# Kernel optimization log

Measured on AMD Instinct MI355X. Metric: run time of the kernel, lower is better.

## Reference

```python
import jax, jax.numpy as jnp
import numpy as np

D_MODEL = 1024
NUM_ATOMS = 16384
TEMPERATURE = 1.0
NEG_INF = -1e9


def setup_inputs() -> dict:
    key = jax.random.key(0)
    kx, kd, km = jax.random.split(key, 3)
    x = jax.random.normal(kx, (4, 2048, D_MODEL), dtype=jnp.float32)
    # xavier_uniform for [num_atoms, d_model]
    limit = float(np.sqrt(6.0 / (NUM_ATOMS + D_MODEL)))
    dictionary = jax.random.uniform(
        kd, (NUM_ATOMS, D_MODEL), dtype=jnp.float32, minval=-limit, maxval=limit
    )
    mask = jax.random.randint(km, (4, 2048, NUM_ATOMS), 0, 2, dtype=jnp.int32)
    return {"x": x, "dictionary": dictionary, "mask": mask}


def reference(x, dictionary, mask):
    # scores: [b, s, num_atoms]
    scores = jnp.einsum("bsd,ad->bsa", x, dictionary)
    m = mask.astype(scores.dtype)
    scores = scores * m + (1.0 - m) * NEG_INF
    weights = jax.nn.softmax(scores / TEMPERATURE, axis=-1)
    reconstruction = jnp.einsum("bsa,ad->bsd", weights, dictionary)
    argmax_indices = jnp.argmax(scores, axis=-1)
    return reconstruction, argmax_indices
```

## Files before the change

### kernel.cpp

```cpp
#include <hip/hip_runtime.h>

#define NTOK   8192
#define DMODEL 1024
#define NATOM  16384

typedef _Float16 half8  __attribute__((ext_vector_type(8)));
typedef _Float16 half4_t __attribute__((ext_vector_type(4)));
typedef float    f32x4  __attribute__((ext_vector_type(4)));

#define GLOAD_LDS16(gsrc, ldst) \
  __builtin_amdgcn_global_load_lds((const __attribute__((address_space(1))) unsigned int*)(gsrc), \
                                   (__attribute__((address_space(3))) unsigned int*)(ldst), 16, 0, 0)

__global__ void cvt_f32_f16(const float* __restrict__ in, _Float16* __restrict__ out, int n4) {
  int i = blockIdx.x * 256 + threadIdx.x;
  if (i >= n4) return;
  float4 v = ((const float4*)in)[i];
  half4_t h;
  h[0] = (_Float16)v.x; h[1] = (_Float16)v.y; h[2] = (_Float16)v.z; h[3] = (_Float16)v.w;
  ((half4_t*)out)[i] = h;
}

__global__ void transpose_dict(const float* __restrict__ dict,
                               _Float16* __restrict__ Dh, _Float16* __restrict__ dT) {
  __shared__ _Float16 tile[64][68];
  int a0 = blockIdx.x * 64;
  int d0 = blockIdx.y * 64;
  int tid = threadIdx.x;
  int c = tid & 63;
  int r0 = tid >> 6;
  #pragma unroll
  for (int i = 0; i < 16; i++) {
    int r = r0 + i * 4;
    _Float16 h = (_Float16)dict[(size_t)(a0 + r) * DMODEL + d0 + c];
    tile[r][c] = h;
    Dh[(size_t)(a0 + r) * DMODEL + d0 + c] = h;
  }
  __syncthreads();
  #pragma unroll
  for (int i = 0; i < 16; i++) {
    int rd = r0 + i * 4;
    dT[(size_t)(d0 + rd) * NATOM + a0 + c] = tile[c][rd];
  }
}

__global__ void zero_lsum(float* __restrict__ lsum) {
  lsum[blockIdx.x * 256 + threadIdx.x] = 0.0f;
}

__device__ __forceinline__ void stage_ab(const _Float16* __restrict__ A,
                                         const _Float16* __restrict__ B,
                                         _Float16* As, _Float16* Bs,
                                         size_t arow0, size_t brow0, size_t ldk,
                                         int k0, int tid) {
  #pragma unroll
  for (int i = 0; i < 2; i++) {
    int L = tid + i * 256;
    int r = L >> 2, pc = L & 3;
    int c = pc ^ ((r >> 1) & 3);
    GLOAD_LDS16(A + (arow0 + r) * ldk + k0 + c * 8, As + (size_t)L * 8);
    GLOAD_LDS16(B + (brow0 + r) * ldk + k0 + c * 8, Bs + (size_t)L * 8);
  }
}

__launch_bounds__(256, 2)
__global__ void score_kernel(const _Float16* __restrict__ Xh,
                             const _Float16* __restrict__ Dh,
                             const int* __restrict__ mask,
                             _Float16* __restrict__ E,
                             float* __restrict__ lsum,
                             _Float16* __restrict__ Tmax) {
  __shared__ _Float16 lds[17408];
  const int tid  = threadIdx.x;
  const int lane = tid & 63;
  const int wave = tid >> 6;
  const int wm = wave >> 1, wn = wave & 1;
  const int m0 = blockIdx.y * 128;
  const int n0 = blockIdx.x * 128;

  const int frow = lane & 15;
  const int fkc  = lane >> 4;

  f32x4 acc[4][4] = {};

  stage_ab(Xh, Dh, lds, lds + 4096, m0, n0, DMODEL, 0, tid);
  int cur = 0;
  for (int it = 0; it < DMODEL / 32; ++it) {
    __syncthreads();
    if (it + 1 < DMODEL / 32)
      stage_ab(Xh, Dh, lds + (cur ^ 1) * 8192, lds + (cur ^ 1) * 8192 + 4096,
               m0, n0, DMODEL, (it + 1) * 32, tid);
    _Float16* As = lds + cur * 8192;
    _Float16* Bs = As + 4096;
    half8 af[4], bf[4];
    #pragma unroll
    for (int i = 0; i < 4; i++) {
      int ar = wm * 64 + i * 16 + frow;
      int br = wn * 64 + i * 16 + frow;
      af[i] = *(const half8*)&As[ar * 32 + (fkc ^ ((ar >> 1) & 3)) * 8];
      bf[i] = *(const half8*)&Bs[br * 32 + (fkc ^ ((br >> 1) & 3)) * 8];
    }
    #pragma unroll
    for (int i = 0; i < 4; i++)
      #pragma unroll
      for (int j = 0; j < 4; j++)
        acc[i][j] = __builtin_amdgcn_mfma_f32_16x16x32_f16(af[i], bf[j], acc[i][j], 0, 0, 0);
    cur ^= 1;
  }

  __syncthreads();
  const int cr = (lane >> 4) * 4;
  const int cc = lane & 15;
  #pragma unroll
  for (int i = 0; i < 4; i++) {
    #pragma unroll
    for (int j = 0; j < 4; j++) {
      #pragma unroll
      for (int r = 0; r < 4; r++) {
        int lr = wm * 64 + i * 16 + cr + r;
        int lc = wn * 64 + j * 16 + cc;
        int mk = mask[(size_t)(m0 + lr) * NATOM + (n0 + lc)];
        float e = mk ? __expf(acc[i][j][r]) : 0.0f;
        lds[lr * 136 + lc] = (_Float16)e;
      }
    }
  }
  __syncthreads();
  #pragma unroll
  for (int i = 0; i < 8; i++) {
    int chunk = i * 256 + tid;
    int r  = chunk >> 4;
    int c8 = (chunk & 15) * 8;
    *(half8*)&E[(size_t)(m0 + r) * NATOM + n0 + c8] = *(const half8*)&lds[r * 136 + c8];
  }
  {
    int r = tid >> 1, h = tid & 1;
    const _Float16* rowp = &lds[r * 136 + h * 64];
    float s = 0.0f, m = 0.0f;
    #pragma unroll
    for (int i = 0; i < 8; i++) {
      half8 v = *(const half8*)&rowp[i * 8];
      #pragma unroll
      for (int j = 0; j < 8; j++) { float f = (float)v[j]; s += f; m = fmaxf(m, f); }
    }
    s += __shfl_xor(s, 1, 64);
    m = fmaxf(m, __shfl_xor(m, 1, 64));
    if (h == 0) {
      atomicAdd(&lsum[m0 + r], s);
      Tmax[(size_t)(m0 + r) * 128 + blockIdx.x] = (_Float16)m;
    }
  }
}

__global__ void scan_lite(const _Float16* __restrict__ E,
                          const _Float16* __restrict__ Tmax,
                          const float* __restrict__ x,
                          const float* __restrict__ dict,
                          float* __restrict__ argout) {
  const int wv   = threadIdx.x >> 6;
  const int lane = threadIdx.x & 63;
  const int t = blockIdx.x * 4 + wv;

  __shared__ int    cnt[4];
  __shared__ int    cand[4][32];
  __shared__ double csc[4][32];
  if (lane == 0) cnt[wv] = 0;

  const _Float16* tm = Tmax + (size_t)t * 128;
  float m0 = (float)tm[lane];
  float m1 = (float)tm[64 + lane];
  float mx = fmaxf(m0, m1);
  #pragma unroll
  for (int off = 32; off > 0; off >>= 1) mx = fmaxf(mx, __shfl_xor(mx, off, 64));

  if (mx > 0.0f) {
    float thr = 0.98f * mx;
    unsigned long long q0 = __ballot(m0 >= thr);
    unsigned long long q1 = __ballot(m1 >= thr);
    while (q0 | q1) {
      int tile;
      if (q0) { tile = __ffsll(q0) - 1; q0 &= q0 - 1; }
      else    { tile = 64 + __ffsll(q1) - 1; q1 &= q1 - 1; }
      const _Float16* ep = E + (size_t)t * NATOM + tile * 128;
      float e0 = (float)ep[lane], e1 = (float)ep[64 + lane];
      if (e0 >= thr) { int p = atomicAdd(&cnt[wv], 1); if (p < 32) cand[wv][p] = tile * 128 + lane; }
      if (e1 >= thr) { int p = atomicAdd(&cnt[wv], 1); if (p < 32) cand[wv][p] = tile * 128 + 64 + lane; }
    }
  }
  int nc = min(cnt[wv], 32);
  const float* xr = x + (size_t)t * DMODEL;
  for (int c = 0; c < nc; c++) {
    const float* dr = dict + (size_t)cand[wv][c] * DMODEL;
    double a = 0.0;
    #pragma unroll
    for (int i = 0; i < 16; i++) {
      int d = lane + i * 64;
      a += (double)xr[d] * (double)dr[d];
    }
    #pragma unroll
    for (int off = 32; off > 0; off >>= 1) a += __shfl_down(a, off, 64);
    if (lane == 0) csc[wv][c] = a;
  }
  if (lane == 0) {
    int best = 0;
    if (nc > 0) {
      double bs = -1e300;
      best = NATOM;
      for (int c = 0; c < nc; c++)
        if (csc[wv][c] > bs || (csc[wv][c] == bs && cand[wv][c] < best)) { bs = csc[wv][c]; best = cand[wv][c]; }
    }
    argout[t] = (float)best;
  }
}

__launch_bounds__(256, 2)
__global__ void recon_kernel(const _Float16* __restrict__ E,
                             const _Float16* __restrict__ DT,
                             const float* __restrict__ lsum,
                             float* __restrict__ out) {
  __shared__ _Float16 lds[32768];
  const int tid  = threadIdx.x;
  const int lane = tid & 63;
  const int wave = tid >> 6;
  const int wm = wave >> 1, wn = wave & 1;
  const int swz = (blockIdx.x & 7) * 64 + (blockIdx.x >> 3);
  const int n0 = (swz & 7) * 128;
  const int m0 = (swz >> 3) * 128;

  const int frow = lane & 15;
  const int fkc  = lane >> 4;

  f32x4 acc[4][4] = {};

  stage_ab(E, DT, lds,         lds + 4096,  m0, n0, NATOM, 0,  tid);
  stage_ab(E, DT, lds + 8192,  lds + 12288, m0, n0, NATOM, 32, tid);
  stage_ab(E, DT, lds + 16384, lds + 20480, m0, n0, NATOM, 64, tid);

  for (int t = 0; t < 512; ++t) {
    if (t < 510)       asm volatile("s_waitcnt vmcnt(8)" ::: "memory");
    else if (t == 510) asm volatile("s_waitcnt vmcnt(4)" ::: "memory");
    else               asm volatile("s_waitcnt vmcnt(0)" ::: "memory");
    __builtin_amdgcn_s_barrier();
    __builtin_amdgcn_sched_barrier(0);
    const _Float16* As = lds + (t & 3) * 8192;
    const _Float16* Bs = As + 4096;
    half8 af[4], bf[4];
    #pragma unroll
    for (int i = 0; i < 4; i++) {
      int ar = wm * 64 + i * 16 + frow;
      int br = wn * 64 + i * 16 + frow;
      af[i] = *(const half8*)&As[ar * 32 + ((fkc ^ ((ar >> 1) & 3)) << 3)];
      bf[i] = *(const half8*)&Bs[br * 32 + ((fkc ^ ((br >> 1) & 3)) << 3)];
    }
    if (t + 3 < 512) {
      int b = (t + 3) & 3;
      stage_ab(E, DT, lds + b * 8192, lds + b * 8192 + 4096, m0, n0, NATOM, (t + 3) * 32, tid);
    }
    __builtin_amdgcn_s_setprio(1);
    #pragma unroll
    for (int i = 0; i < 4; i++)
      #pragma unroll
      for (int j = 0; j < 4; j++)
        acc[i][j] = __builtin_amdgcn_mfma_f32_16x16x32_f16(af[i], bf[j], acc[i][j], 0, 0, 0);
    __builtin_amdgcn_s_setprio(0);
    __builtin_amdgcn_sched_barrier(0);
  }

  const int cr = (lane >> 4) * 4;
  const int cc = lane & 15;
  #pragma unroll
  for (int i = 0; i < 4; i++) {
    #pragma unroll
    for (int r = 0; r < 4; r++) {
      int lr = wm * 64 + i * 16 + cr + r;
      float sc = 1.0f / lsum[m0 + lr];
      #pragma unroll
      for (int j = 0; j < 4; j++) {
        int lc = wn * 64 + j * 16 + cc;
        out[(size_t)(m0 + lr) * DMODEL + (n0 + lc)] = acc[i][j][r] * sc;
      }
    }
  }
}

extern "C" void kernel_launch(void* const* d_in, const int* in_sizes, int n_in,
                              void* d_out, int out_size, void* d_ws, size_t ws_size,
                              hipStream_t stream) {
  const float* x    = (const float*)d_in[0];
  const float* dict = (const float*)d_in[1];
  const int*   mask = (const int*)d_in[2];
  float* recon  = (float*)d_out;
  float* argout = recon + (size_t)NTOK * DMODEL;

  char* w = (char*)d_ws;
  _Float16* Xh = (_Float16*)(w);
  _Float16* Dh = (_Float16*)(w + (size_t)16  * 1024 * 1024);
  _Float16* DT = (_Float16*)(w + (size_t)48  * 1024 * 1024);
  _Float16* E  = (_Float16*)(w + (size_t)80  * 1024 * 1024);
  float*  lsum = (float*)  (w + (size_t)336 * 1024 * 1024);
  _Float16* Tmax = (_Float16*)d_out;

  cvt_f32_f16<<<dim3(NTOK * DMODEL / 4 / 256), 256, 0, stream>>>(x, Xh, NTOK * DMODEL / 4);
  transpose_dict<<<dim3(NATOM / 64, DMODEL / 64), 256, 0, stream>>>(dict, Dh, DT);
  zero_lsum<<<dim3(NTOK / 256), 256, 0, stream>>>(lsum);
  score_kernel<<<dim3(NATOM / 128, NTOK / 128), 256, 0, stream>>>(Xh, Dh, mask, E, lsum, Tmax);
  scan_lite<<<dim3(NTOK / 4), 256, 0, stream>>>(E, Tmax, x, dict, argout);
  recon_kernel<<<dim3(512), 256, 0, stream>>>(E, DT, lsum, recon);
}
```

Before: 1.426 ms.

## Enlarge score GEMM tile to 256x256 with 8 waves and interleaved async staging

The score GEMM moves from 128x128 tiles with 4 waves to 256x256 tiles with 8 waves and a K-step of 64. Each K-tile is split into sub-stages whose global-to-LDS loads are issued between MFMA groups, with explicit waitcnt, barriers, sched_barrier and setprio to overlap loads with compute. The aim is more operand reuse per loaded byte and fewer sync stalls. The cost is 128 KB of LDS per block and more accumulator registers, which may limit occupancy. The epilogue now writes out in two 128-column halves.

```diff
diff --git a/kernel.cpp b/kernel.cpp
--- a/kernel.cpp
+++ b/kernel.cpp
@@ -63,93 +63,174 @@
   }
 }
 
-__launch_bounds__(256, 2)
+__device__ __forceinline__ void stage_item(const _Float16* __restrict__ src, int row0,
+                                           int kt, int s, _Float16* dst, int tid) {
+  #pragma unroll
+  for (int i = 0; i < 2; i++) {
+    int L2 = tid + i * 512;
+    int r = L2 >> 2, q = L2 & 3;
+    int c = s * 4 + (q ^ (r & 3));
+    GLOAD_LDS16(src + (size_t)(row0 + r) * DMODEL + kt * 64 + c * 8, dst + (size_t)L2 * 8);
+  }
+}
+
+__launch_bounds__(512, 2)
 __global__ void score_kernel(const _Float16* __restrict__ Xh,
                              const _Float16* __restrict__ Dh,
                              const int* __restrict__ mask,
                              _Float16* __restrict__ E,
                              float* __restrict__ lsum,
                              _Float16* __restrict__ Tmax) {
-  __shared__ _Float16 lds[17408];
+  __shared__ _Float16 lds[65536];
   const int tid  = threadIdx.x;
   const int lane = tid & 63;
   const int wave = tid >> 6;
-  const int wm = wave >> 1, wn = wave & 1;
-  const int m0 = blockIdx.y * 128;
-  const int n0 = blockIdx.x * 128;
+  const int wm = wave >> 2;
+  const int wn = wave & 3;
+  const int m0 = blockIdx.y * 256;
+  const int n0 = blockIdx.x * 256;
 
   const int frow = lane & 15;
   const int fkc  = lane >> 4;
 
-  f32x4 acc[4][4] = {};
-
-  stage_ab(Xh, Dh, lds, lds + 4096, m0, n0, DMODEL, 0, tid);
-  int cur = 0;
-  for (int it = 0; it < DMODEL / 32; ++it) {
-    __syncthreads();
-    if (it + 1 < DMODEL / 32)
-      stage_ab(Xh, Dh, lds + (cur ^ 1) * 8192, lds + (cur ^ 1) * 8192 + 4096,
-               m0, n0, DMODEL, (it + 1) * 32, tid);
-    _Float16* As = lds + cur * 8192;
-    _Float16* Bs = As + 4096;
+  f32x4 acc[8][4] = {};
+
+  #define AOFF(B_, S_, ROW_) ((B_) * 32768 + (S_) * 8192 + (((ROW_) << 2) + (fkc ^ ((ROW_) & 3))) * 8)
+  #define BOFF(B_, S_, ROW_) ((B_) * 32768 + 16384 + (S_) * 8192 + (((ROW_) << 2) + (fkc ^ ((ROW_) & 3))) * 8)
+
+  stage_item(Xh, m0, 0, 0, lds,         tid);
+  stage_item(Dh, n0, 0, 0, lds + 16384, tid);
+  stage_item(Xh, m0, 0, 1, lds + 8192,  tid);
+  stage_item(Dh, n0, 0, 1, lds + 24576, tid);
+  asm volatile("s_waitcnt vmcnt(4)" ::: "memory");
+  __builtin_amdgcn_s_barrier();
+
+  const int NKT = DMODEL / 64;
+  for (int kt = 0; kt < NKT; ++kt) {
+    const int b  = kt & 1;
+    const int nb = b ^ 1;
+    const bool more = (kt + 1 < NKT);
     half8 af[4], bf[4];
-    #pragma unroll
-    for (int i = 0; i < 4; i++) {
-      int ar = wm * 64 + i * 16 + frow;
-      int br = wn * 64 + i * 16 + frow;
-      af[i] = *(const half8*)&As[ar * 32 + (fkc ^ ((ar >> 1) & 3)) * 8];
-      bf[i] = *(const half8*)&Bs[br * 32 + (fkc ^ ((br >> 1) & 3)) * 8];
-    }
+
+    #pragma unroll
+    for (int i = 0; i < 4; i++) af[i] = *(const half8*)&lds[AOFF(b, 0, wm * 128 + i * 16 + frow)];
+    #pragma unroll
+    for (int j = 0; j < 4; j++) bf[j] = *(const half8*)&lds[BOFF(b, 0, wn * 64 + j * 16 + frow)];
+    if (more) stage_item(Xh, m0, kt + 1, 0, lds + nb * 32768, tid);
+    asm volatile("s_waitcnt lgkmcnt(0)" ::: "memory");
+    __builtin_amdgcn_sched_barrier(0);
+    __builtin_amdgcn_s_setprio(1);
     #pragma unroll
     for (int i = 0; i < 4; i++)
       #pragma unroll
       for (int j = 0; j < 4; j++)
         acc[i][j] = __builtin_amdgcn_mfma_f32_16x16x32_f16(af[i], bf[j], acc[i][j], 0, 0, 0);
-    cur ^= 1;
-  }
-
-  __syncthreads();
+    __builtin_amdgcn_s_setprio(0);
+    __builtin_amdgcn_sched_barrier(0);
+    __builtin_amdgcn_s_barrier();
+
+    #pragma unroll
+    for (int i = 0; i < 4; i++) af[i] = *(const half8*)&lds[AOFF(b, 0, wm * 128 + 64 + i * 16 + frow)];
+    if (more) stage_item(Dh, n0, kt + 1, 0, lds + nb * 32768 + 16384, tid);
+    asm volatile("s_waitcnt lgkmcnt(0)" ::: "memory");
+    __builtin_amdgcn_sched_barrier(0);
+    __builtin_amdgcn_s_setprio(1);
+    #pragma unroll
+    for (int i = 0; i < 4; i++)
+      #pragma unroll
+      for (int j = 0; j < 4; j++)
+        acc[4 + i][j] = __builtin_amdgcn_mfma_f32_16x16x32_f16(af[i], bf[j], acc[4 + i][j], 0, 0, 0);
+    __builtin_amdgcn_s_setprio(0);
+    __builtin_amdgcn_sched_barrier(0);
+    if (more) asm volatile("s_waitcnt vmcnt(4)" ::: "memory");
+    else      asm volatile("s_waitcnt vmcnt(0)" ::: "memory");
+    __builtin_amdgcn_s_barrier();
+
+    #pragma unroll
+    for (int i = 0; i < 4; i++) af[i] = *(const half8*)&lds[AOFF(b, 1, wm * 128 + i * 16 + frow)];
+    #pragma unroll
+    for (int j = 0; j < 4; j++) bf[j] = *(const half8*)&lds[BOFF(b, 1, wn * 64 + j * 16 + frow)];
+    if (more) stage_item(Xh, m0, kt + 1, 1, lds + nb * 32768 + 8192, tid);
+    asm volatile("s_waitcnt lgkmcnt(0)" ::: "memory");
+    __builtin_amdgcn_sched_barrier(0);
+    __builtin_amdgcn_s_setprio(1);
+    #pragma unroll
+    for (int i = 0; i < 4; i++)
+      #pragma unroll
+      for (int j = 0; j < 4; j++)
+        acc[i][j] = __builtin_amdgcn_mfma_f32_16x16x32_f16(af[i], bf[j], acc[i][j], 0, 0, 0);
+    __builtin_amdgcn_s_setprio(0);
+    __builtin_amdgcn_sched_barrier(0);
+    __builtin_amdgcn_s_barrier();
+
+    #pragma unroll
+    for (int i = 0; i < 4; i++) af[i] = *(const half8*)&lds[AOFF(b, 1, wm * 128 + 64 + i * 16 + frow)];
+    if (more) stage_item(Dh, n0, kt + 1, 1, lds + nb * 32768 + 24576, tid);
+    asm volatile("s_waitcnt lgkmcnt(0)" ::: "memory");
+    __builtin_amdgcn_sched_barrier(0);
+    __builtin_amdgcn_s_setprio(1);
+    #pragma unroll
+    for (int i = 0; i < 4; i++)
+      #pragma unroll
+      for (int j = 0; j < 4; j++)
+        acc[4 + i][j] = __builtin_amdgcn_mfma_f32_16x16x32_f16(af[i], bf[j], acc[4 + i][j], 0, 0, 0);
+    __builtin_amdgcn_s_setprio(0);
+    __builtin_amdgcn_sched_barrier(0);
+    if (more) asm volatile("s_waitcnt vmcnt(4)" ::: "memory");
+    __builtin_amdgcn_s_barrier();
+  }
+  #undef AOFF
+  #undef BOFF
+
   const int cr = (lane >> 4) * 4;
   const int cc = lane & 15;
-  #pragma unroll
-  for (int i = 0; i < 4; i++) {
-    #pragma unroll
-    for (int j = 0; j < 4; j++) {
-      #pragma unroll
-      for (int r = 0; r < 4; r++) {
-        int lr = wm * 64 + i * 16 + cr + r;
-        int lc = wn * 64 + j * 16 + cc;
-        int mk = mask[(size_t)(m0 + lr) * NATOM + (n0 + lc)];
-        float e = mk ? __expf(acc[i][j][r]) : 0.0f;
-        lds[lr * 136 + lc] = (_Float16)e;
+  const int rr = tid >> 1, hh = tid & 1;
+  float s_acc = 0.0f;
+  #pragma unroll
+  for (int h = 0; h < 2; h++) {
+    if ((wn >> 1) == h) {
+      #pragma unroll
+      for (int i = 0; i < 8; i++) {
+        #pragma unroll
+        for (int j = 0; j < 4; j++) {
+          #pragma unroll
+          for (int r = 0; r < 4; r++) {
+            int lr = wm * 128 + i * 16 + cr + r;
+            int lc = (wn & 1) * 64 + j * 16 + cc;
+            int mk = mask[(size_t)(m0 + lr) * NATOM + n0 + h * 128 + lc];
+            float e = mk ? __expf(acc[i][j][r]) : 0.0f;
+            lds[lr * 136 + lc] = (_Float16)e;
+          }
+        }
       }
     }
-  }
-  __syncthreads();
-  #pragma unroll
-  for (int i = 0; i < 8; i++) {
-    int chunk = i * 256 + tid;
-    int r  = chunk >> 4;
-    int c8 = (chunk & 15) * 8;
-    *(half8*)&E[(size_t)(m0 + r) * NATOM + n0 + c8] = *(const half8*)&lds[r * 136 + c8];
-  }
-  {
-    int r = tid >> 1, h = tid & 1;
-    const _Float16* rowp = &lds[r * 136 + h * 64];
-    float s = 0.0f, m = 0.0f;
+    __builtin_amdgcn_s_barrier();
     #pragma unroll
     for (int i = 0; i < 8; i++) {
-      half8 v = *(const half8*)&rowp[i * 8];
-      #pragma unroll
-      for (int j = 0; j < 8; j++) { float f = (float)v[j]; s += f; m = fmaxf(m, f); }
-    }
-    s += __shfl_xor(s, 1, 64);
-    m = fmaxf(m, __shfl_xor(m, 1, 64));
-    if (h == 0) {
-      atomicAdd(&lsum[m0 + r], s);
-      Tmax[(size_t)(m0 + r) * 128 + blockIdx.x] = (_Float16)m;
-    }
-  }
+      int chunk = i * 512 + tid;
+      int r  = chunk >> 4;
+      int c8 = (chunk & 15) * 8;
+      *(half8*)&E[(size_t)(m0 + r) * NATOM + n0 + h * 128 + c8] = *(const half8*)&lds[r * 136 + c8];
+    }
+    {
+      const _Float16* rowp = &lds[rr * 136 + hh * 64];
+      float s = 0.0f, m = 0.0f;
+      #pragma unroll
+      for (int i = 0; i < 8; i++) {
+        half8 v = *(const half8*)&rowp[i * 8];
+        #pragma unroll
+        for (int j = 0; j < 8; j++) { float f = (float)v[j]; s += f; m = fmaxf(m, f); }
+      }
+      s += __shfl_xor(s, 1, 64);
+      m = fmaxf(m, __shfl_xor(m, 1, 64));
+      if (hh == 0) {
+        s_acc += s;
+        Tmax[(size_t)(m0 + rr) * 128 + blockIdx.x * 2 + h] = (_Float16)m;
+      }
+    }
+    __builtin_amdgcn_s_barrier();
+  }
+  if (hh == 0) atomicAdd(&lsum[m0 + rr], s_acc);
 }
 
 __global__ void scan_lite(const _Float16* __restrict__ E,
@@ -303,7 +384,7 @@
   cvt_f32_f16<<<dim3(NTOK * DMODEL / 4 / 256), 256, 0, stream>>>(x, Xh, NTOK * DMODEL / 4);
   transpose_dict<<<dim3(NATOM / 64, DMODEL / 64), 256, 0, stream>>>(dict, Dh, DT);
   zero_lsum<<<dim3(NTOK / 256), 256, 0, stream>>>(lsum);
-  score_kernel<<<dim3(NATOM / 128, NTOK / 128), 256, 0, stream>>>(Xh, Dh, mask, E, lsum, Tmax);
+  score_kernel<<<dim3(NATOM / 256, NTOK / 256), 512, 0, stream>>>(Xh, Dh, mask, E, lsum, Tmax);
   scan_lite<<<dim3(NTOK / 4), 256, 0, stream>>>(E, Tmax, x, dict, argout);
   recon_kernel<<<dim3(512), 256, 0, stream>>>(E, DT, lsum, recon);
 }
```

Result: faster. 1.379 ms (-3.3%).
